# Kernel optimization log

Measured on AMD Instinct MI355X. Metric: run time of the kernel, lower is better.

Reference implementation:

```python
import jax, jax.numpy as jnp
import numpy as np

LEVEL_SHAPES = ((100, 100), (50, 50), (25, 25))  # (H, W) per feature level
B, S, D, H, L, P, FFN = 2, 13125, 256, 8, 3, 4, 1024
Dh = D // H


def setup_inputs() -> dict:
    key = jax.random.key(0)
    ks = jax.random.split(key, 24)

    def rn(k, shape, s=0.02):
        return jax.random.normal(k, shape, jnp.float32) * s

    starts = np.cumsum([0] + [h * w for h, w in LEVEL_SHAPES])[:-1]
    return {
        "x": jax.random.normal(ks[0], (B, S, D), jnp.float32),
        "pos_embed": jax.random.normal(ks[1], (B, S, D), jnp.float32) * 0.1,
        "ref_points": jax.random.uniform(ks[2], (B, S, L, 2), jnp.float32),
        "W_off": rn(ks[3], (D, H * L * P * 2)),
        "b_off": rn(ks[4], (H * L * P * 2,), 0.5),
        "W_attn": rn(ks[5], (D, H * L * P)),
        "b_attn": rn(ks[6], (H * L * P,)),
        "W_val": rn(ks[7], (D, D)),
        "b_val": rn(ks[8], (D,)),
        "W_out": rn(ks[9], (D, D)),
        "b_out": rn(ks[10], (D,)),
        "g1": jnp.ones((D,), jnp.float32),
        "be1": jnp.zeros((D,), jnp.float32),
        "W1": rn(ks[11], (D, FFN)),
        "b1": rn(ks[12], (FFN,)),
        "W2": rn(ks[13], (FFN, D)),
        "b2": rn(ks[14], (D,)),
        "g2": jnp.ones((D,), jnp.float32),
        "be2": jnp.zeros((D,), jnp.float32),
        "level_shapes": jnp.array(LEVEL_SHAPES, jnp.int32),
        "level_start_idx": jnp.array(starts, jnp.int32),
    }


def layer_norm(x, g, b, eps=1e-5):
    m = jnp.mean(x, -1, keepdims=True)
    v = jnp.var(x, -1, keepdims=True)
    return (x - m) * jax.lax.rsqrt(v + eps) * g + b


def bilinear_sample(vl, loc, Hl, Wl):
    # vl: [B,H,S_l,Dh]; loc: [B,H,S,P,2] normalized (x,y) in [0,1]
    # grid_sample semantics: align_corners=False, padding_mode='zeros'
    x = loc[..., 0] * Wl - 0.5
    y = loc[..., 1] * Hl - 0.5
    x0 = jnp.floor(x)
    y0 = jnp.floor(y)
    fx = x - x0
    fy = y - y0
    x0i = x0.astype(jnp.int32)
    y0i = y0.astype(jnp.int32)
    out = 0.0
    for dy, dx, w in ((0, 0, (1 - fx) * (1 - fy)), (0, 1, fx * (1 - fy)),
                      (1, 0, (1 - fx) * fy), (1, 1, fx * fy)):
        xi = x0i + dx
        yi = y0i + dy
        valid = (xi >= 0) & (xi < Wl) & (yi >= 0) & (yi < Hl)
        idx = jnp.clip(yi, 0, Hl - 1) * Wl + jnp.clip(xi, 0, Wl - 1)
        b_, h_, s_, p_ = idx.shape
        g = jnp.take_along_axis(vl, idx.reshape(b_, h_, s_ * p_)[..., None], axis=2)
        g = g.reshape(b_, h_, s_, p_, Dh)
        out = out + g * (w * valid)[..., None]
    return out  # [B,H,S,P,Dh]


def ms_deform_attn(q, x, ref_points, W_off, b_off, W_attn, b_attn, W_val, b_val, W_out, b_out):
    value = (x @ W_val + b_val).reshape(B, S, H, Dh).transpose(0, 2, 1, 3)  # [B,H,S,Dh]
    off = (q @ W_off + b_off).reshape(B, S, H, L, P, 2)
    attn = jax.nn.softmax((q @ W_attn + b_attn).reshape(B, S, H, L * P), axis=-1)
    attn = attn.reshape(B, S, H, L, P).transpose(0, 2, 1, 3, 4)  # [B,H,S,L,P]
    # offset normalizer is (W, H) per level
    norm = jnp.array([[w, h] for h, w in LEVEL_SHAPES], jnp.float32)
    loc = ref_points[:, :, None, :, None, :] + off / norm[None, None, None, :, None, :]
    loc = loc.transpose(0, 2, 1, 3, 4, 5)  # [B,H,S,L,P,2]
    s0 = 0
    sampled = []
    for l, (Hl, Wl) in enumerate(LEVEL_SHAPES):
        vl = jax.lax.slice_in_dim(value, s0, s0 + Hl * Wl, axis=2)
        sampled.append(bilinear_sample(vl, loc[:, :, :, l], Hl, Wl))
        s0 += Hl * Wl
    sampled = jnp.stack(sampled, axis=3)  # [B,H,S,L,P,Dh]
    out = jnp.einsum('bhslp,bhslpd->bshd', attn, sampled).reshape(B, S, D)
    return out @ W_out + b_out


def reference(x, pos_embed, ref_points, W_off, b_off, W_attn, b_attn, W_val, b_val,
              W_out, b_out, g1, be1, W1, b1, W2, b2, g2, be2,
              level_shapes, level_start_idx):
    q = x + pos_embed
    attn_out = ms_deform_attn(q, x, ref_points, W_off, b_off, W_attn, b_attn,
                              W_val, b_val, W_out, b_out)
    h1 = layer_norm(x + attn_out, g1, be1)
    ffn = jax.nn.relu(h1 @ W1 + b1) @ W2 + b2
    return layer_norm(h1 + ffn, g2, be2)
```

## Files before the change

### kernel.cpp

```cpp
#include <hip/hip_runtime.h>
#include <hip/hip_bf16.h>

namespace {

constexpr int kB = 2, kS = 13125, kD = 256, kH = 8, kL = 3, kP = 4, kFFN = 1024, kDh = 32;
constexpr int kM = kB * kS;

typedef __attribute__((ext_vector_type(8))) short short8v;
typedef __attribute__((ext_vector_type(4))) float f32x4;
typedef __attribute__((ext_vector_type(2))) float f32x2;
typedef __attribute__((ext_vector_type(2))) unsigned int uint2v;

__device__ __forceinline__ float bf2f(unsigned short u) {
  unsigned int x = ((unsigned int)u) << 16;
  return __builtin_bit_cast(float, x);
}
__device__ __forceinline__ unsigned short f2bf(float f) {
  unsigned int u = __builtin_bit_cast(unsigned int, f);
  u += 0x7FFFu + ((u >> 16) & 1u);
  return (unsigned short)(u >> 16);
}

__device__ __forceinline__ void gload_lds16(const void* g, void* l) {
  __builtin_amdgcn_global_load_lds(
      (const __attribute__((address_space(1))) unsigned int*)g,
      (__attribute__((address_space(3))) unsigned int*)l, 16, 0, 0);
}

__global__ __launch_bounds__(256) void wprep_kernel(const float* __restrict__ W,
                                                    unsigned short* __restrict__ Wt,
                                                    int K, int N, int total) {
  int idx = blockIdx.x * 256 + threadIdx.x;
  if (idx >= total) return;
  int n = idx / K, k = idx - n * K;
  float v = (n < N) ? W[(size_t)k * N + n] : 0.f;
  Wt[idx] = f2bf(v);
}

__global__ __launch_bounds__(256) void wprep_comb(const float* __restrict__ Woff,
                                                  const float* __restrict__ Wattn,
                                                  const float* __restrict__ boff,
                                                  const float* __restrict__ battn,
                                                  unsigned short* __restrict__ Wt,
                                                  float* __restrict__ bc) {
  int idx = blockIdx.x * 256 + threadIdx.x;
  if (idx >= 288 * 256) return;
  int n = idx >> 8, k = idx & 255;
  int h = n / 36, j = n - h * 36;
  float v = (j < 24) ? Woff[(size_t)k * 192 + h * 24 + j]
                     : Wattn[(size_t)k * 96 + h * 12 + (j - 24)];
  Wt[idx] = f2bf(v);
  if (idx < 288) {
    int hh = idx / 36, jj = idx - hh * 36;
    bc[idx] = (jj < 24) ? boff[hh * 24 + jj] : battn[hh * 12 + (jj - 24)];
  }
}

__global__ __launch_bounds__(256) void prep_kernel(const float4* __restrict__ x,
                                                   const float4* __restrict__ pos,
                                                   ushort4* __restrict__ xb,
                                                   ushort4* __restrict__ qb, int n4) {
  int i = blockIdx.x * 256 + threadIdx.x;
  if (i < n4) {
    float4 a = x[i], b = pos[i];
    xb[i] = make_ushort4(f2bf(a.x), f2bf(a.y), f2bf(a.z), f2bf(a.w));
    qb[i] = make_ushort4(f2bf(a.x + b.x), f2bf(a.y + b.y),
                         f2bf(a.z + b.z), f2bf(a.w + b.w));
  }
}

template <int EPI, bool OBF, int MI, bool VHM>
__global__ __launch_bounds__(256) void mfma_gemm(const unsigned short* __restrict__ A,
                                                 const unsigned short* __restrict__ Bt,
                                                 const float* __restrict__ bias,
                                                 void* __restrict__ Cp,
                                                 int M, int N, int K) {
  constexpr int BM = MI * 32;
  __shared__ unsigned short smem[2 * 128 * 32];
  unsigned short* As = smem;
  unsigned short* Bs = smem + BM * 32;
  const int tid = threadIdx.x;
  const int w = tid >> 6, lane = tid & 63;
  const int m0 = blockIdx.y * BM, n0 = blockIdx.x * 128;
  const int wr = w >> 1, wc = w & 1;
  const int r_ = lane >> 2, sl = lane & 3;

  f32x4 acc[MI][4] = {};

  for (int k0 = 0; k0 < K; k0 += 32) {
#pragma unroll
    for (int i = 0; i < MI / 2; ++i) {
      const int row = i * 64 + w * 16 + r_;
      const int sg = sl ^ ((row >> 1) & 3);
      int arow = m0 + row;
      arow = arow < M ? arow : M - 1;
      gload_lds16(A + (size_t)arow * K + k0 + sg * 8, &As[(i * 64 + w * 16) * 32]);
    }
#pragma unroll
    for (int i = 0; i < 2; ++i) {
      const int row = i * 64 + w * 16 + r_;
      const int sg = sl ^ ((row >> 1) & 3);
      gload_lds16(Bt + (size_t)(n0 + row) * K + k0 + sg * 8, &Bs[(i * 64 + w * 16) * 32]);
    }
    __syncthreads();
    short8v a[MI], b[4];
#pragma unroll
    for (int mi = 0; mi < MI; ++mi) {
      const int row = wr * (MI * 16) + mi * 16 + (lane & 15);
      const int slot = (lane >> 4) ^ ((row >> 1) & 3);
      a[mi] = *(const short8v*)&As[row * 32 + slot * 8];
    }
#pragma unroll
    for (int ni = 0; ni < 4; ++ni) {
      const int row = wc * 64 + ni * 16 + (lane & 15);
      const int slot = (lane >> 4) ^ ((row >> 1) & 3);
      b[ni] = *(const short8v*)&Bs[row * 32 + slot * 8];
    }
#pragma unroll
    for (int mi = 0; mi < MI; ++mi)
#pragma unroll
      for (int ni = 0; ni < 4; ++ni)
        acc[mi][ni] = __builtin_amdgcn_mfma_f32_16x16x32_bf16(a[mi], b[ni], acc[mi][ni], 0, 0, 0);
    __syncthreads();
  }

  const int cr = lane >> 4, cc = lane & 15;
  if (OBF) {
    unsigned short* Cs = smem;
#pragma unroll
    for (int half = 0; half < MI / 2; ++half) {
      if (MI == 2 || wr == half) {
#pragma unroll
        for (int ni = 0; ni < 4; ++ni) {
          const int col = wc * 64 + ni * 16 + cc;
          const float bv = bias[n0 + col];
#pragma unroll
          for (int mi = 0; mi < MI; ++mi)
#pragma unroll
            for (int r = 0; r < 4; ++r) {
              const int loc = wr * (MI * 16) + mi * 16 + cr * 4 + r - half * 64;
              float v = acc[mi][ni][r] + bv;
              if (EPI == 2) v = fmaxf(v, 0.f);
              const int ch = (col >> 3) ^ (loc & 7);
              Cs[loc * 128 + ch * 8 + (col & 7)] = f2bf(v);
            }
        }
      }
      __syncthreads();
      const int lr = tid >> 4, lc = tid & 15;
#pragma unroll
      for (int pp = 0; pp < 4; ++pp) {
        const int loc = pp * 16 + lr;
        const int grow = m0 + half * 64 + loc;
        const short8v vv = *(const short8v*)&Cs[loc * 128 + ((lc ^ (loc & 7)) * 8)];
        if (grow < M) {
          if (VHM) {
            const int col = n0 + lc * 8;
            const int bb = grow >= kS ? 1 : 0;
            const int ss = grow - bb * kS;
            const int hh = col >> 5;
            *(short8v*)((unsigned short*)Cp +
                        (((size_t)(bb * kH + hh) * kS + ss) * kDh + (col & 31))) = vv;
          } else {
            *(short8v*)((unsigned short*)Cp + (size_t)grow * N + n0 + lc * 8) = vv;
          }
        }
      }
      __syncthreads();
    }
  } else {
#pragma unroll
    for (int ni = 0; ni < 4; ++ni) {
      const int col = n0 + wc * 64 + ni * 16 + cc;
      if (col >= N) continue;
      const float bv = bias[col];
#pragma unroll
      for (int mi = 0; mi < MI; ++mi) {
#pragma unroll
        for (int r = 0; r < 4; ++r) {
          const int row = m0 + wr * (MI * 16) + mi * 16 + cr * 4 + r;
          if (row >= M) continue;
          ((float*)Cp)[(size_t)row * N + col] = acc[mi][ni][r] + bv;
        }
      }
    }
  }
}

__global__ __launch_bounds__(512, 4) void ffn_fused(const unsigned short* __restrict__ Ain,
                                                    const unsigned short* __restrict__ W1t,
                                                    const unsigned short* __restrict__ W2t,
                                                    const float* __restrict__ b1,
                                                    const float* __restrict__ b2,
                                                    unsigned short* __restrict__ Cp,
                                                    int M) {
  __shared__ unsigned short W1s[2][64 * 256];
  __shared__ unsigned short Ps[2 * 64 * 32];
  const int tid = threadIdx.x;
  const int w = tid >> 6, lane = tid & 63;
  const int m0 = blockIdx.x * 64;
  const int cr = lane >> 4, cc = lane & 15;
  const int mw = w & 3;
  const int fw = w >> 2;

  short8v areg[8];
  {
    int grow = m0 + mw * 16 + cc;
    grow = grow < M ? grow : M - 1;
    const unsigned short* ap = Ain + (size_t)grow * 256 + cr * 8;
#pragma unroll
    for (int kk = 0; kk < 8; ++kk) areg[kk] = *(const short8v*)(ap + kk * 32);
  }

  auto stage_w1 = [&](int jt, int buf) {
    const unsigned short* src = W1t + (size_t)jt * 64 * 256;
#pragma unroll
    for (int it = 0; it < 4; ++it) {
      const int idx = it * 512 + tid;
      const int kk = idx >> 8;
      const int row = (idx >> 2) & 63;
      const int sl = idx & 3;
      const int ssl = sl ^ ((row >> 1) & 3);
      gload_lds16(src + (size_t)row * 256 + kk * 32 + ssl * 8, &W1s[buf][idx * 8]);
    }
  };

  f32x4 acc[4][2] = {};

  stage_w1(0, 0);
  __syncthreads();

  for (int jt = 0; jt < 16; ++jt) {
    const int buf = jt & 1;
    if (jt < 15) stage_w1(jt + 1, buf ^ 1);

    f32x4 p1[2] = {};
#pragma unroll
    for (int kk = 0; kk < 8; ++kk) {
#pragma unroll
      for (int lf = 0; lf < 2; ++lf) {
        const int row = fw * 32 + lf * 16 + cc;
        const short8v wv = *(const short8v*)
            &W1s[buf][kk * 2048 + row * 32 + ((cr ^ ((row >> 1) & 3)) * 8)];
        p1[lf] = __builtin_amdgcn_mfma_f32_16x16x32_bf16(wv, areg[kk], p1[lf], 0, 0, 0);
      }
    }
    {
      const int row = mw * 16 + cc;
      const int rsw = (row >> 1) & 3;
#pragma unroll
      for (int lf = 0; lf < 2; ++lf) {
        const float4 bv = *(const float4*)&b1[jt * 64 + fw * 32 + lf * 16 + cr * 4];
        const unsigned int u0 =
            (unsigned)f2bf(fmaxf(p1[lf][0] + bv.x, 0.f)) |
            ((unsigned)f2bf(fmaxf(p1[lf][1] + bv.y, 0.f)) << 16);
        const unsigned int u1 =
            (unsigned)f2bf(fmaxf(p1[lf][2] + bv.z, 0.f)) |
            ((unsigned)f2bf(fmaxf(p1[lf][3] + bv.w, 0.f)) << 16);
        const int slot = lf * 2 + (cr >> 1);
        uint2v* dst = (uint2v*)&Ps[fw * 2048 + row * 32 + ((slot ^ rsw) * 8) + (cr & 1) * 4];
        *dst = (uint2v){u0, u1};
      }
    }
    __syncthreads();

#pragma unroll
    for (int kk2 = 0; kk2 < 2; ++kk2) {
      short8v pf[4];
#pragma unroll
      for (int mi = 0; mi < 4; ++mi) {
        const int row = mi * 16 + cc;
        pf[mi] = *(const short8v*)
            &Ps[kk2 * 2048 + row * 32 + ((cr ^ ((row >> 1) & 3)) * 8)];
      }
#pragma unroll
      for (int ni = 0; ni < 2; ++ni) {
        const int ncol = w * 32 + ni * 16 + cc;
        const short8v wv =
            *(const short8v*)(W2t + (size_t)ncol * 1024 + jt * 64 + kk2 * 32 + cr * 8);
#pragma unroll
        for (int mi = 0; mi < 4; ++mi)
          acc[mi][ni] = __builtin_amdgcn_mfma_f32_16x16x32_bf16(pf[mi], wv, acc[mi][ni], 0, 0, 0);
      }
    }
    __syncthreads();
  }

  unsigned short* Cs = &W1s[0][0];
#pragma unroll
  for (int ni = 0; ni < 2; ++ni) {
    const int col = w * 32 + ni * 16 + cc;
    const float bv = b2[col];
#pragma unroll
    for (int mi = 0; mi < 4; ++mi)
#pragma unroll
      for (int r = 0; r < 4; ++r) {
        const int row = mi * 16 + cr * 4 + r;
        const float v = acc[mi][ni][r] + bv;
        Cs[row * 256 + (((col >> 3) ^ (row & 7)) * 8) + (col & 7)] = f2bf(v);
      }
  }
  __syncthreads();
#pragma unroll
  for (int it = 0; it < 4; ++it) {
    const int row = it * 16 + (tid >> 5);
    const int grow = m0 + row;
    const int ch = tid & 31;
    const short8v vv = *(const short8v*)&Cs[row * 256 + ((ch ^ (row & 7)) * 8)];
    if (grow < M) *(short8v*)(Cp + (size_t)grow * 256 + ch * 8) = vv;
  }
}

__device__ __forceinline__ void acc2u(f32x2* acc, unsigned u, int i, float m) {
  f32x2 v;
  v.x = __builtin_bit_cast(float, u << 16);
  v.y = __builtin_bit_cast(float, u & 0xFFFF0000u);
  acc[i] += m * v;
}
__device__ __forceinline__ void acc_corner(f32x2* acc, uint4 q, float m) {
  acc2u(acc, q.x, 0, m);
  acc2u(acc, q.y, 1, m);
  acc2u(acc, q.z, 2, m);
  acc2u(acc, q.w, 3, m);
}

__global__ __launch_bounds__(256) void sample_kernel(const unsigned short* __restrict__ value,
                                                     const float* __restrict__ oa,
                                                     const float* __restrict__ refp,
                                                     unsigned short* __restrict__ out) {
  const int tid = threadIdx.x;
  const int sub = tid >> 2;
  const int lane = tid & 3;
  const int gi = blockIdx.x * 64 + sub;
  if (gi >= kB * kS * kH) return;
  const int h = gi & 7;
  const int bs = gi >> 3;
  const int b = (bs >= kS) ? 1 : 0;

  const float* op = oa + (size_t)bs * 288 + h * 36;
  const float* al = op + 24;
  float w[12];
  float mx = -1e30f;
#pragma unroll
  for (int i = 0; i < 12; ++i) { w[i] = al[i]; mx = fmaxf(mx, w[i]); }
  float sum = 0.f;
#pragma unroll
  for (int i = 0; i < 12; ++i) { w[i] = __expf(w[i] - mx); sum += w[i]; }
  const float inv = 1.f / sum;
#pragma unroll
  for (int i = 0; i < 12; ++i) w[i] *= inv;

  const float* rp = refp + (size_t)bs * (kL * 2);
  const unsigned short* vbase = value + ((size_t)(b * kH + h) * kS) * kDh + lane * 8;

  const int LH[3] = {100, 50, 25}, LW[3] = {100, 50, 25}, LS[3] = {0, 10000, 12500};
  f32x2 acc[4] = {};
#pragma unroll
  for (int l = 0; l < 3; ++l) {
    const int Wi = LW[l], Hi = LH[l];
    const float Wl = (float)Wi, Hl = (float)Hi;
    const float rxw = rp[l * 2 + 0] * Wl - 0.5f;
    const float ryh = rp[l * 2 + 1] * Hl - 0.5f;
    const unsigned short* lvl = vbase + (size_t)LS[l] * kDh;
#pragma unroll
    for (int p = 0; p < 4; ++p) {
      const float ox = op[l * 8 + p * 2 + 0], oy = op[l * 8 + p * 2 + 1];
      const float xf = rxw + ox;
      const float yf = ryh + oy;
      const float x0f = floorf(xf), y0f = floorf(yf);
      const float fx = xf - x0f, fy = yf - y0f;
      const int x0 = (int)x0f, y0 = (int)y0f;
      const int x1 = x0 + 1, y1 = y0 + 1;
      const bool vx0 = (unsigned)x0 < (unsigned)Wi;
      const bool vx1 = (unsigned)x1 < (unsigned)Wi;
      const bool vy0 = (unsigned)y0 < (unsigned)Hi;
      const bool vy1 = (unsigned)y1 < (unsigned)Hi;
      const int cx0 = min(max(x0, 0), Wi - 1), cx1 = min(max(x1, 0), Wi - 1);
      const int cy0 = min(max(y0, 0), Hi - 1), cy1 = min(max(y1, 0), Hi - 1);
      const float aw = w[l * 4 + p];
      const float ax = aw * fx, a0 = aw - ax;
      const float w00 = a0 - a0 * fy, w10 = a0 * fy;
      const float w01 = ax - ax * fy, w11 = ax * fy;
      const float m00 = (vx0 && vy0) ? w00 : 0.f;
      const float m01 = (vx1 && vy0) ? w01 : 0.f;
      const float m10 = (vx0 && vy1) ? w10 : 0.f;
      const float m11 = (vx1 && vy1) ? w11 : 0.f;
      const int ry0 = cy0 * Wi, ry1 = cy1 * Wi;
      const uint4 q00 = *(const uint4*)(lvl + (size_t)(ry0 + cx0) * kDh);
      const uint4 q01 = *(const uint4*)(lvl + (size_t)(ry0 + cx1) * kDh);
      const uint4 q10 = *(const uint4*)(lvl + (size_t)(ry1 + cx0) * kDh);
      const uint4 q11 = *(const uint4*)(lvl + (size_t)(ry1 + cx1) * kDh);
      acc_corner(acc, q00, m00);
      acc_corner(acc, q01, m01);
      acc_corner(acc, q10, m10);
      acc_corner(acc, q11, m11);
    }
  }
  unsigned short r[8];
#pragma unroll
  for (int i = 0; i < 4; ++i) {
    r[2 * i] = f2bf(acc[i].x);
    r[2 * i + 1] = f2bf(acc[i].y);
  }
  *(short8v*)(out + (size_t)bs * kD + h * kDh + lane * 8) = *(const short8v*)r;
}

template <int WB>
__global__ __launch_bounds__(256) void lnres_kernel(const float* __restrict__ X,
                                                    const unsigned short* __restrict__ Ab,
                                                    const float* __restrict__ g,
                                                    const float* __restrict__ be,
                                                    float* __restrict__ out,
                                                    unsigned short* __restrict__ outb,
                                                    int rows) {
  const int wid = threadIdx.x >> 6, lane = threadIdx.x & 63;
  const int row = blockIdx.x * 4 + wid;
  if (row >= rows) return;
  const float4 v = ((const float4*)(X + (size_t)row * kD))[lane];
  const ushort4 a4 = ((const ushort4*)(Ab + (size_t)row * kD))[lane];
  float4 t;
  t.x = v.x + bf2f(a4.x);
  t.y = v.y + bf2f(a4.y);
  t.z = v.z + bf2f(a4.z);
  t.w = v.w + bf2f(a4.w);
  float s = t.x + t.y + t.z + t.w;
  float sq = t.x * t.x + t.y * t.y + t.z * t.z + t.w * t.w;
#pragma unroll
  for (int o = 1; o < 64; o <<= 1) {
    s += __shfl_xor(s, o);
    sq += __shfl_xor(sq, o);
  }
  const float mean = s * (1.f / kD);
  const float var = sq * (1.f / kD) - mean * mean;
  const float rs = rsqrtf(var + 1e-5f);
  const float4 gg = ((const float4*)g)[lane];
  const float4 bb = ((const float4*)be)[lane];
  float4 o4;
  o4.x = (t.x - mean) * rs * gg.x + bb.x;
  o4.y = (t.y - mean) * rs * gg.y + bb.y;
  o4.z = (t.z - mean) * rs * gg.z + bb.z;
  o4.w = (t.w - mean) * rs * gg.w + bb.w;
  ((float4*)(out + (size_t)row * kD))[lane] = o4;
  if (WB) {
    ((ushort4*)(outb + (size_t)row * kD))[lane] =
        make_ushort4(f2bf(o4.x), f2bf(o4.y), f2bf(o4.z), f2bf(o4.w));
  }
}

}

extern "C" void kernel_launch(void* const* d_in, const int* in_sizes, int n_in,
                              void* d_out, int out_size, void* d_ws, size_t ws_size,
                              hipStream_t stream) {
  const float* x      = (const float*)d_in[0];
  const float* pos    = (const float*)d_in[1];
  const float* refp   = (const float*)d_in[2];
  const float* W_off  = (const float*)d_in[3];
  const float* b_off  = (const float*)d_in[4];
  const float* W_attn = (const float*)d_in[5];
  const float* b_attn = (const float*)d_in[6];
  const float* W_val  = (const float*)d_in[7];
  const float* b_val  = (const float*)d_in[8];
  const float* W_out  = (const float*)d_in[9];
  const float* b_out  = (const float*)d_in[10];
  const float* g1     = (const float*)d_in[11];
  const float* be1    = (const float*)d_in[12];
  const float* W1     = (const float*)d_in[13];
  const float* b1     = (const float*)d_in[14];
  const float* W2     = (const float*)d_in[15];
  const float* b2     = (const float*)d_in[16];
  const float* g2     = (const float*)d_in[17];
  const float* be2    = (const float*)d_in[18];
  float* outp = (float*)d_out;

  char* ws = (char*)d_ws;
  unsigned short* Wvt = (unsigned short*)(ws + 0);
  unsigned short* Wot = (unsigned short*)(ws + 131072);
  unsigned short* Wct = (unsigned short*)(ws + 262144);
  float* bcomb        = (float*)(ws + 262144 + 288 * 512);
  unsigned short* W1t = (unsigned short*)(ws + 458752);
  unsigned short* W2t = (unsigned short*)(ws + 983040);
  const size_t MDb = (size_t)kM * kD * 2;
  char* regA = ws + 1507328;
  char* regB = regA + MDb;
  char* regC = regB + MDb;
  char* regG = regC + 43680000;

  unsigned short* xb    = (unsigned short*)regA;
  unsigned short* aob   = (unsigned short*)regA;
  unsigned short* qb    = (unsigned short*)regB;
  unsigned short* f2b   = (unsigned short*)regB;
  unsigned short* value = (unsigned short*)regC;
  float* oa   = (float*)(regC + MDb);
  float* h1   = (float*)regC;
  unsigned short* h1b = (unsigned short*)(regC + (size_t)kM * kD * 4);
  unsigned short* sv  = (unsigned short*)regG;

  const dim3 blk(256);
  const int mt64 = (kM + 63) / 64;
  const int n4 = kM * kD / 4;

  wprep_kernel<<<(256 * 256 + 255) / 256, blk, 0, stream>>>(W_val, Wvt, 256, 256, 256 * 256);
  wprep_kernel<<<(256 * 256 + 255) / 256, blk, 0, stream>>>(W_out, Wot, 256, 256, 256 * 256);
  wprep_comb<<<288, blk, 0, stream>>>(W_off, W_attn, b_off, b_attn, Wct, bcomb);
  wprep_kernel<<<(1024 * 256 + 255) / 256, blk, 0, stream>>>(W1, W1t, 256, 1024, 1024 * 256);
  wprep_kernel<<<(256 * 1024 + 255) / 256, blk, 0, stream>>>(W2, W2t, 1024, 256, 256 * 1024);

  prep_kernel<<<(n4 + 255) / 256, blk, 0, stream>>>((const float4*)x, (const float4*)pos,
                                                    (ushort4*)xb, (ushort4*)qb, n4);
  mfma_gemm<0, true, 2, true><<<dim3(2, mt64), blk, 0, stream>>>(xb, Wvt, b_val, value,
                                                                 kM, 256, 256);
  mfma_gemm<0, false, 2, false><<<dim3(3, mt64), blk, 0, stream>>>(qb, Wct, bcomb, oa,
                                                                   kM, 288, 256);
  sample_kernel<<<(kB * kS * kH + 63) / 64, blk, 0, stream>>>(value, oa, refp, sv);
  mfma_gemm<0, true, 2, false><<<dim3(2, mt64), blk, 0, stream>>>(sv, Wot, b_out, aob,
                                                                  kM, 256, 256);
  lnres_kernel<1><<<(kM + 3) / 4, blk, 0, stream>>>(x, aob, g1, be1, h1, h1b, kM);
  ffn_fused<<<mt64, dim3(512), 0, stream>>>(h1b, W1t, W2t, b1, b2, f2b, kM);
  lnres_kernel<0><<<(kM + 3) / 4, blk, 0, stream>>>(h1, f2b, g2, be2, outp, nullptr, kM);
}
```

Measured before the change: 206.7 us.

## Software-pipeline FFN second GEMM with double-buffered P and merge weight-prep kernels

The fused FFN kernel now double-buffers the intermediate activation tile in shared memory. It computes the second GEMM for the previous tile while producing the current one, which removes one block-wide barrier per iteration, and it fully unrolls the tile loop. Separately, the five weight transpose/convert launches are merged into one kernel to cut launch overhead. The cost is extra LDS (8 KB) and higher register pressure from the unroll, which may reduce occupancy.

Result: faster. 197.2 us (-4.6%).

```diff
diff --git a/kernel.cpp b/kernel.cpp
--- a/kernel.cpp
+++ b/kernel.cpp
@@ -27,32 +27,47 @@
       (__attribute__((address_space(3))) unsigned int*)l, 16, 0, 0);
 }
 
-__global__ __launch_bounds__(256) void wprep_kernel(const float* __restrict__ W,
-                                                    unsigned short* __restrict__ Wt,
-                                                    int K, int N, int total) {
+__global__ __launch_bounds__(256) void wprep_all(const float* __restrict__ Wv,
+                                                 const float* __restrict__ Wo,
+                                                 const float* __restrict__ Woff,
+                                                 const float* __restrict__ Wattn,
+                                                 const float* __restrict__ boff,
+                                                 const float* __restrict__ battn,
+                                                 const float* __restrict__ W1,
+                                                 const float* __restrict__ W2,
+                                                 unsigned short* __restrict__ Wvt,
+                                                 unsigned short* __restrict__ Wot,
+                                                 unsigned short* __restrict__ Wct,
+                                                 float* __restrict__ bcomb,
+                                                 unsigned short* __restrict__ W1t,
+                                                 unsigned short* __restrict__ W2t) {
   int idx = blockIdx.x * 256 + threadIdx.x;
-  if (idx >= total) return;
-  int n = idx / K, k = idx - n * K;
-  float v = (n < N) ? W[(size_t)k * N + n] : 0.f;
-  Wt[idx] = f2bf(v);
-}
-
-__global__ __launch_bounds__(256) void wprep_comb(const float* __restrict__ Woff,
-                                                  const float* __restrict__ Wattn,
-                                                  const float* __restrict__ boff,
-                                                  const float* __restrict__ battn,
-                                                  unsigned short* __restrict__ Wt,
-                                                  float* __restrict__ bc) {
-  int idx = blockIdx.x * 256 + threadIdx.x;
-  if (idx >= 288 * 256) return;
-  int n = idx >> 8, k = idx & 255;
-  int h = n / 36, j = n - h * 36;
-  float v = (j < 24) ? Woff[(size_t)k * 192 + h * 24 + j]
-                     : Wattn[(size_t)k * 96 + h * 12 + (j - 24)];
-  Wt[idx] = f2bf(v);
-  if (idx < 288) {
-    int hh = idx / 36, jj = idx - hh * 36;
-    bc[idx] = (jj < 24) ? boff[hh * 24 + jj] : battn[hh * 12 + (jj - 24)];
+  if (idx < 65536) {
+    int n = idx >> 8, k = idx & 255;
+    Wvt[idx] = f2bf(Wv[k * 256 + n]);
+  } else if (idx < 131072) {
+    int j = idx - 65536;
+    int n = j >> 8, k = j & 255;
+    Wot[j] = f2bf(Wo[k * 256 + n]);
+  } else if (idx < 204800) {
+    int j = idx - 131072;
+    int n = j >> 8, k = j & 255;
+    int h = n / 36, jj = n - h * 36;
+    float v = (jj < 24) ? Woff[(size_t)k * 192 + h * 24 + jj]
+                        : Wattn[(size_t)k * 96 + h * 12 + (jj - 24)];
+    Wct[j] = f2bf(v);
+    if (j < 288) {
+      int hh = j / 36, q = j - hh * 36;
+      bcomb[j] = (q < 24) ? boff[hh * 24 + q] : battn[hh * 12 + (q - 24)];
+    }
+  } else if (idx < 466944) {
+    int j = idx - 204800;
+    int n = j >> 8, k = j & 255;
+    W1t[j] = f2bf(W1[(size_t)k * 1024 + n]);
+  } else if (idx < 729088) {
+    int j = idx - 466944;
+    int n = j >> 10, k = j & 1023;
+    W2t[j] = f2bf(W2[(size_t)k * 256 + n]);
   }
 }
 
@@ -195,7 +210,7 @@
                                                     unsigned short* __restrict__ Cp,
                                                     int M) {
   __shared__ unsigned short W1s[2][64 * 256];
-  __shared__ unsigned short Ps[2 * 64 * 32];
+  __shared__ unsigned short Ps[2][2 * 64 * 32];
   const int tid = threadIdx.x;
   const int w = tid >> 6, lane = tid & 63;
   const int m0 = blockIdx.x * 64;
@@ -230,6 +245,7 @@
   stage_w1(0, 0);
   __syncthreads();
 
+#pragma unroll
   for (int jt = 0; jt < 16; ++jt) {
     const int buf = jt & 1;
     if (jt < 15) stage_w1(jt + 1, buf ^ 1);
@@ -258,12 +274,38 @@
             (unsigned)f2bf(fmaxf(p1[lf][2] + bv.z, 0.f)) |
             ((unsigned)f2bf(fmaxf(p1[lf][3] + bv.w, 0.f)) << 16);
         const int slot = lf * 2 + (cr >> 1);
-        uint2v* dst = (uint2v*)&Ps[fw * 2048 + row * 32 + ((slot ^ rsw) * 8) + (cr & 1) * 4];
+        uint2v* dst = (uint2v*)&Ps[buf][fw * 2048 + row * 32 + ((slot ^ rsw) * 8) + (cr & 1) * 4];
         *dst = (uint2v){u0, u1};
       }
     }
+
+    if (jt > 0) {
+      const unsigned short* Pr = Ps[buf ^ 1];
+#pragma unroll
+      for (int kk2 = 0; kk2 < 2; ++kk2) {
+        short8v pf[4];
+#pragma unroll
+        for (int mi = 0; mi < 4; ++mi) {
+          const int row = mi * 16 + cc;
+          pf[mi] = *(const short8v*)
+              &Pr[kk2 * 2048 + row * 32 + ((cr ^ ((row >> 1) & 3)) * 8)];
+        }
+#pragma unroll
+        for (int ni = 0; ni < 2; ++ni) {
+          const int ncol = w * 32 + ni * 16 + cc;
+          const short8v wv = *(const short8v*)
+              (W2t + (size_t)ncol * 1024 + (jt - 1) * 64 + kk2 * 32 + cr * 8);
+#pragma unroll
+          for (int mi = 0; mi < 4; ++mi)
+            acc[mi][ni] = __builtin_amdgcn_mfma_f32_16x16x32_bf16(pf[mi], wv, acc[mi][ni], 0, 0, 0);
+        }
+      }
+    }
     __syncthreads();
-
+  }
+
+  {
+    const unsigned short* Pr = Ps[1];
 #pragma unroll
     for (int kk2 = 0; kk2 < 2; ++kk2) {
       short8v pf[4];
@@ -271,20 +313,20 @@
       for (int mi = 0; mi < 4; ++mi) {
         const int row = mi * 16 + cc;
         pf[mi] = *(const short8v*)
-            &Ps[kk2 * 2048 + row * 32 + ((cr ^ ((row >> 1) & 3)) * 8)];
+            &Pr[kk2 * 2048 + row * 32 + ((cr ^ ((row >> 1) & 3)) * 8)];
       }
 #pragma unroll
       for (int ni = 0; ni < 2; ++ni) {
         const int ncol = w * 32 + ni * 16 + cc;
-        const short8v wv =
-            *(const short8v*)(W2t + (size_t)ncol * 1024 + jt * 64 + kk2 * 32 + cr * 8);
+        const short8v wv = *(const short8v*)
+            (W2t + (size_t)ncol * 1024 + 15 * 64 + kk2 * 32 + cr * 8);
 #pragma unroll
         for (int mi = 0; mi < 4; ++mi)
           acc[mi][ni] = __builtin_amdgcn_mfma_f32_16x16x32_bf16(pf[mi], wv, acc[mi][ni], 0, 0, 0);
       }
     }
-    __syncthreads();
-  }
+  }
+  __syncthreads();
 
   unsigned short* Cs = &W1s[0][0];
 #pragma unroll
@@ -500,12 +542,9 @@
   const int mt64 = (kM + 63) / 64;
   const int n4 = kM * kD / 4;
 
-  wprep_kernel<<<(256 * 256 + 255) / 256, blk, 0, stream>>>(W_val, Wvt, 256, 256, 256 * 256);
-  wprep_kernel<<<(256 * 256 + 255) / 256, blk, 0, stream>>>(W_out, Wot, 256, 256, 256 * 256);
-  wprep_comb<<<288, blk, 0, stream>>>(W_off, W_attn, b_off, b_attn, Wct, bcomb);
-  wprep_kernel<<<(1024 * 256 + 255) / 256, blk, 0, stream>>>(W1, W1t, 256, 1024, 1024 * 256);
-  wprep_kernel<<<(256 * 1024 + 255) / 256, blk, 0, stream>>>(W2, W2t, 1024, 256, 256 * 1024);
-
+  wprep_all<<<(729088 + 255) / 256, blk, 0, stream>>>(W_val, W_out, W_off, W_attn,
+                                                      b_off, b_attn, W1, W2,
+                                                      Wvt, Wot, Wct, bcomb, W1t, W2t);
   prep_kernel<<<(n4 + 255) / 256, blk, 0, stream>>>((const float4*)x, (const float4*)pos,
                                                     (ushort4*)xb, (ushort4*)qb, n4);
   mfma_gemm<0, true, 2, true><<<dim3(2, mt64), blk, 0, stream>>>(xb, Wvt, b_val, value,
```
